# Kernel optimization log

Hardware: AMD Instinct MI355X
Metric: run time of the kernel (lower is better)

## Reference

```python
import jax, jax.numpy as jnp
import numpy as np

K = 2
CAPACITY_FACTOR = 1.25


def setup_inputs() -> dict:
    key = jax.random.key(0)
    ks = jax.random.split(key, 5)
    B, T, D, F, E = 4, 2048, 1024, 4096, 8
    x = jax.random.normal(ks[0], (B, T, D), dtype=jnp.float32)
    w_gate = jax.random.normal(ks[1], (E, D), dtype=jnp.float32) * (1.0 / np.sqrt(D))
    W1 = jax.random.normal(ks[2], (E, F, D), dtype=jnp.float32) * np.sqrt(2.0 / (D + F))
    b1 = jnp.zeros((E, F), dtype=jnp.float32)
    W2 = jax.random.normal(ks[3], (E, D, F), dtype=jnp.float32) * np.sqrt(2.0 / (D + F))
    b2 = jnp.zeros((E, D), dtype=jnp.float32)
    return {"x": x, "w_gate": w_gate, "W1": W1, "b1": b1, "W2": W2, "b2": b2}


def reference(x, w_gate, W1, b1, W2, b2):
    B, T, D = x.shape
    E = w_gate.shape[0]
    S = B * T
    C = int(CAPACITY_FACTOR * S * K / E)  # per-expert capacity
    tokens = x.reshape(S, D)

    # --- routing (fp32 softmax, top-k) ---
    logits = tokens @ w_gate.T                      # [S, E]
    probs = jax.nn.softmax(logits, axis=-1)         # [S, E]
    topk_vals, topk_idx = jax.lax.top_k(probs, K)   # [S, K]

    e_flat = topk_idx.reshape(-1)                   # [S*K] expert id per assignment
    g_flat = topk_vals.reshape(-1)                  # [S*K] gate value
    t_flat = jnp.repeat(jnp.arange(S), K)           # [S*K] source token index

    # --- capacity: position of each assignment within its expert (arrival order) ---
    onehot = jax.nn.one_hot(e_flat, E, dtype=jnp.int32)       # [S*K, E]
    pos = jnp.sum(jnp.cumsum(onehot, axis=0) * onehot, axis=-1) - 1  # [S*K]
    keep = pos < C

    # --- dispatch into [E, C, D] buffer (over-capacity assignments dropped) ---
    buf = jnp.zeros((E, C, D), dtype=tokens.dtype).at[e_flat, pos].set(
        tokens[t_flat], mode="drop")

    # --- grouped expert FFN: fc2(gelu(fc1(x))) + x  (exact gelu, as torch F.gelu) ---
    h = jax.nn.gelu(jnp.einsum("ecd,efd->ecf", buf, W1) + b1[:, None, :],
                    approximate=False)              # [E, C, F]
    expert_out = jnp.einsum("ecf,edf->ecd", h, W2) + b2[:, None, :] + buf  # [E, C, D]

    # --- combine: scatter-add gate-weighted expert outputs back to tokens ---
    gathered = expert_out[e_flat, jnp.clip(pos, 0, C - 1)]    # [S*K, D]
    w = jnp.where(keep, g_flat, 0.0)[:, None]
    y = jnp.zeros((S, D), dtype=tokens.dtype).at[t_flat].add(w * gathered)

    # --- load-balancing aux loss ---
    importance = probs.mean(axis=0)                            # [E]
    counts = jnp.zeros((E,), dtype=probs.dtype).at[e_flat].add(1.0)
    load = counts / S
    aux_loss = E * jnp.sum(importance * load)

    return y.reshape(B, T, D), aux_loss
```

## Files before the change

kernel.cpp:

```cpp
#include <hip/hip_runtime.h>
#include <hip/hip_bf16.h>
#include <math.h>
#include <stdint.h>

#define S_TOK 8192
#define D_DIM 1024
#define F_DIM 4096
#define E_EXP 8
#define C_CAP 2560

typedef __bf16 bf16x8_t __attribute__((ext_vector_type(8)));
typedef __bf16 bf16x4_t __attribute__((ext_vector_type(4)));
typedef float f32x4_t __attribute__((ext_vector_type(4)));

__device__ __forceinline__ void async_copy16(const void* g, void* l) {
  __builtin_amdgcn_global_load_lds(
      (const __attribute__((address_space(1))) unsigned int*)g,
      (__attribute__((address_space(3))) unsigned int*)l, 16, 0, 0);
}

__global__ __launch_bounds__(256) void routing_kernel(
    const float* __restrict__ x, const float* __restrict__ wg,
    __bf16* __restrict__ x_bf, int* __restrict__ asg_e, float* __restrict__ asg_g,
    float* __restrict__ imp_sum)
{
  __shared__ float s_imp[E_EXP];
  const int tid = threadIdx.x, lane = tid & 63, w = tid >> 6;
  if (tid < E_EXP) s_imp[tid] = 0.f;
  __syncthreads();
  const int t = blockIdx.x * 4 + w;

  const float4* xp = (const float4*)(x + (size_t)t * D_DIM);
  float4 xv[4];
#pragma unroll
  for (int j = 0; j < 4; j++) xv[j] = xp[lane + 64 * j];

#pragma unroll
  for (int j = 0; j < 4; j++) {
    bf16x4_t o;
    o[0] = (__bf16)xv[j].x; o[1] = (__bf16)xv[j].y;
    o[2] = (__bf16)xv[j].z; o[3] = (__bf16)xv[j].w;
    *(bf16x4_t*)(x_bf + (size_t)t * D_DIM + (size_t)(lane + 64 * j) * 4) = o;
  }

  float acc[E_EXP];
#pragma unroll
  for (int e = 0; e < E_EXP; e++) acc[e] = 0.f;
#pragma unroll
  for (int e = 0; e < E_EXP; e++) {
    const float4* wp = (const float4*)(wg + (size_t)e * D_DIM);
#pragma unroll
    for (int j = 0; j < 4; j++) {
      const float4 wv = wp[lane + 64 * j];
      acc[e] += xv[j].x * wv.x + xv[j].y * wv.y + xv[j].z * wv.z + xv[j].w * wv.w;
    }
  }
#pragma unroll
  for (int e = 0; e < E_EXP; e++)
    for (int off = 32; off > 0; off >>= 1) acc[e] += __shfl_xor(acc[e], off);

  if (lane == 0) {
    float m = acc[0];
#pragma unroll
    for (int e = 1; e < E_EXP; e++) m = fmaxf(m, acc[e]);
    float p[E_EXP], s = 0.f;
#pragma unroll
    for (int e = 0; e < E_EXP; e++) { p[e] = expf(acc[e] - m); s += p[e]; }
    const float inv = 1.f / s;
#pragma unroll
    for (int e = 0; e < E_EXP; e++) p[e] *= inv;
    int e0 = 0; float v0 = p[0];
#pragma unroll
    for (int e = 1; e < E_EXP; e++) if (p[e] > v0) { v0 = p[e]; e0 = e; }
    int e1 = -1; float v1 = -1.f;
#pragma unroll
    for (int e = 0; e < E_EXP; e++) if (e != e0 && p[e] > v1) { v1 = p[e]; e1 = e; }
    asg_e[2 * t] = e0; asg_g[2 * t] = v0;
    asg_e[2 * t + 1] = e1; asg_g[2 * t + 1] = v1;
#pragma unroll
    for (int e = 0; e < E_EXP; e++) atomicAdd(&s_imp[e], p[e]);
  }
  __syncthreads();
  if (tid < E_EXP) atomicAdd(&imp_sum[tid], s_imp[tid]);
}

__global__ __launch_bounds__(256) void cvt2_kernel(
    const float* __restrict__ s1, const float* __restrict__ s2,
    __bf16* __restrict__ d1, __bf16* __restrict__ d2, int n4each)
{
  const int stride = gridDim.x * blockDim.x;
  for (int i = blockIdx.x * blockDim.x + threadIdx.x; i < 2 * n4each; i += stride) {
    const int half = (i >= n4each);
    const int j = half ? (i - n4each) : i;
    const float4 v = half ? ((const float4*)s2)[j] : ((const float4*)s1)[j];
    bf16x4_t o;
    o[0] = (__bf16)v.x; o[1] = (__bf16)v.y; o[2] = (__bf16)v.z; o[3] = (__bf16)v.w;
    if (half) ((bf16x4_t*)d2)[j] = o; else ((bf16x4_t*)d1)[j] = o;
  }
}

__global__ __launch_bounds__(256) void positions_kernel(
    const int* __restrict__ asg_e, const float* __restrict__ asg_g,
    const float* __restrict__ imp_sum, int* __restrict__ slot_token,
    float* __restrict__ slot_gate, int* __restrict__ cnt_g, float* __restrict__ aux_out)
{
  __shared__ int lcnt[E_EXP * 256];
  __shared__ int tot[E_EXP];
  const int tid = threadIdx.x;
  int cnt[E_EXP];
#pragma unroll
  for (int e = 0; e < E_EXP; e++) cnt[e] = 0;
  const int a0 = tid * 64;
  for (int j = 0; j < 64; j++) {
    const int ae = asg_e[a0 + j];
#pragma unroll
    for (int e = 0; e < E_EXP; e++) cnt[e] += (ae == e) ? 1 : 0;
  }
#pragma unroll
  for (int e = 0; e < E_EXP; e++) lcnt[e * 256 + tid] = cnt[e];
  __syncthreads();
  if (tid < E_EXP) {
    int run = 0;
    for (int i = 0; i < 256; i++) { const int v = lcnt[tid * 256 + i]; lcnt[tid * 256 + i] = run; run += v; }
    tot[tid] = run;
    cnt_g[tid] = run;
  }
  __syncthreads();
  int base[E_EXP];
#pragma unroll
  for (int e = 0; e < E_EXP; e++) base[e] = lcnt[e * 256 + tid];
  for (int j = 0; j < 64; j++) {
    const int a = a0 + j;
    const int ae = asg_e[a];
    int pp = 0;
#pragma unroll
    for (int e = 0; e < E_EXP; e++) {
      if (ae == e) { pp = base[e]; base[e] = pp + 1; }
    }
    if (pp < C_CAP) { slot_token[ae * C_CAP + pp] = a >> 1; slot_gate[ae * C_CAP + pp] = asg_g[a]; }
  }
  if (tid == 0) {
    float aux = 0.f;
#pragma unroll
    for (int e = 0; e < E_EXP; e++) aux += imp_sum[e] * (float)tot[e];
    aux_out[0] = (float)E_EXP * aux / ((float)S_TOK * (float)S_TOK);
  }
}

#define WAIT_VM0 asm volatile("s_waitcnt vmcnt(0)" ::: "memory")

template <int MODE>
__global__ __launch_bounds__(256, 2) void moe_gemm(
    const __bf16* __restrict__ A, const __bf16* __restrict__ Bw,
    const float* __restrict__ bias, const int* __restrict__ slot_token,
    const float* __restrict__ slot_gate, const float* __restrict__ xres,
    const int* __restrict__ cnt, __bf16* __restrict__ Hout, float* __restrict__ y,
    int MT, int NT, int N, int K)
{
  const int ntiles = gridDim.x;
  const int xcd = blockIdx.x & 7, slot = blockIdx.x >> 3;
  const int tile = xcd * (ntiles >> 3) + slot;
  const int e = tile / (MT * NT);
  const int t_ = tile % (MT * NT);
  const int grp = t_ / (4 * NT), rem = t_ % (4 * NT);
  const int mt = grp * 4 + (rem & 3), nt = rem >> 2;
  const int m0 = mt * 128, n0 = nt * 128;
  if (m0 >= cnt[e]) return;

  const int tid = threadIdx.x, lane = tid & 63, w = tid >> 6;
  const int wm = w >> 1, wn = w & 1;

  __shared__ __align__(16) unsigned short sA[2][128][64];
  __shared__ __align__(16) unsigned short sB[2][128][64];

  const int rstage = lane >> 3;
  const int cstage = (lane & 7) ^ rstage;

  const char* gA[4];
  const char* gB[4];
#pragma unroll
  for (int i = 0; i < 4; i++) {
    const int rowA = w * 32 + i * 8 + rstage;
    size_t arow;
    if (MODE == 0) {
      int tok = slot_token[e * C_CAP + m0 + rowA];
      if (tok < 0) tok = 0;
      arow = (size_t)tok * (size_t)K;
    } else {
      arow = ((size_t)(e * C_CAP + m0 + rowA)) * (size_t)K;
    }
    gA[i] = (const char*)(A + arow) + cstage * 16;
    const int rowB = w * 32 + i * 8 + rstage;
    const size_t brow = ((size_t)(e * N + n0 + rowB)) * (size_t)K;
    gB[i] = (const char*)(Bw + brow) + cstage * 16;
  }

#define STAGE(BUF, kt) do {                                                         \
    const size_t koff_ = (size_t)(kt) * 128;                                        \
    _Pragma("unroll")                                                               \
    for (int i_ = 0; i_ < 4; i_++)                                                  \
      async_copy16(gA[i_] + koff_, (void*)&sA[BUF][w * 32 + i_ * 8][0]);            \
    _Pragma("unroll")                                                               \
    for (int i_ = 0; i_ < 4; i_++)                                                  \
      async_copy16(gB[i_] + koff_, (void*)&sB[BUF][w * 32 + i_ * 8][0]);            \
  } while (0)

  f32x4_t acc[4][4];
#pragma unroll
  for (int mi = 0; mi < 4; mi++)
#pragma unroll
    for (int ni = 0; ni < 4; ni++) acc[mi][ni] = (f32x4_t){0.f, 0.f, 0.f, 0.f};

  const int fr = lane & 15;
  const int fq = lane >> 4;

#define COMPUTE(BUF)                                                                \
  _Pragma("unroll")                                                                 \
  for (int kk = 0; kk < 2; kk++) {                                                  \
    bf16x8_t af[4], bfv[4];                                                         \
    _Pragma("unroll")                                                               \
    for (int mi = 0; mi < 4; mi++) {                                                \
      const int row = wm * 64 + mi * 16 + fr;                                       \
      const int chk = (kk * 4 + fq) ^ (row & 7);                                    \
      af[mi] = *(const bf16x8_t*)&sA[BUF][row][chk * 8];                            \
    }                                                                               \
    _Pragma("unroll")                                                               \
    for (int ni = 0; ni < 4; ni++) {                                                \
      const int row = wn * 64 + ni * 16 + fr;                                       \
      const int chk = (kk * 4 + fq) ^ (row & 7);                                    \
      bfv[ni] = *(const bf16x8_t*)&sB[BUF][row][chk * 8];                           \
    }                                                                               \
    __builtin_amdgcn_s_setprio(1);                                                  \
    _Pragma("unroll")                                                               \
    for (int mi = 0; mi < 4; mi++)                                                  \
      _Pragma("unroll")                                                             \
      for (int ni = 0; ni < 4; ni++)                                                \
        acc[mi][ni] = __builtin_amdgcn_mfma_f32_16x16x32_bf16(af[mi], bfv[ni],      \
                                                              acc[mi][ni], 0, 0, 0);\
    __builtin_amdgcn_s_setprio(0);                                                  \
  }

  const int NTILES = K >> 6;
  STAGE(0, 0);
  WAIT_VM0;
  __builtin_amdgcn_s_barrier();

  for (int t = 0; t < NTILES; t += 2) {
    STAGE(1, t + 1);
    COMPUTE(0);
    WAIT_VM0;
    __builtin_amdgcn_s_barrier();
    if (t + 2 < NTILES) {
      STAGE(0, t + 2);
      COMPUTE(1);
      WAIT_VM0;
      __builtin_amdgcn_s_barrier();
    } else {
      COMPUTE(1);
    }
  }

  const int col_lo = lane & 15;
  const int row_hi = (lane >> 4) * 4;
  if (MODE == 0) {
#pragma unroll
    for (int ni = 0; ni < 4; ni++) {
      const int gcol = n0 + wn * 64 + ni * 16 + col_lo;
      const float bv = bias[e * N + gcol];
#pragma unroll
      for (int mi = 0; mi < 4; mi++) {
#pragma unroll
        for (int r = 0; r < 4; r++) {
          const int grow = m0 + wm * 64 + mi * 16 + row_hi + r;
          const float v = acc[mi][ni][r] + bv;
          const float gl = 0.5f * v * (1.0f + erff(v * 0.70710678118654752f));
          Hout[((size_t)(e * C_CAP + grow)) * (size_t)N + gcol] = (__bf16)gl;
        }
      }
    }
  } else {
#pragma unroll
    for (int mi = 0; mi < 4; mi++) {
#pragma unroll
      for (int r = 0; r < 4; r++) {
        const int slotI = e * C_CAP + m0 + wm * 64 + mi * 16 + row_hi + r;
        const int tok = slot_token[slotI];
        if (tok < 0) continue;
        const float g = slot_gate[slotI];
        const size_t trow = (size_t)tok * (size_t)N;
#pragma unroll
        for (int ni = 0; ni < 4; ni++) {
          const int gcol = n0 + wn * 64 + ni * 16 + col_lo;
          const float v = acc[mi][ni][r] + bias[e * N + gcol] + xres[trow + gcol];
          atomicAdd(&y[trow + gcol], g * v);
        }
      }
    }
  }
#undef STAGE
#undef COMPUTE
}

extern "C" void kernel_launch(void* const* d_in, const int* in_sizes, int n_in,
                              void* d_out, int out_size, void* d_ws, size_t ws_size,
                              hipStream_t stream) {
  const float* x  = (const float*)d_in[0];
  const float* wg = (const float*)d_in[1];
  const float* W1 = (const float*)d_in[2];
  const float* b1 = (const float*)d_in[3];
  const float* W2 = (const float*)d_in[4];
  const float* b2 = (const float*)d_in[5];
  float* y = (float*)d_out;

  char* p = (char*)d_ws;
  __bf16* x_bf = (__bf16*)p;    p += (size_t)S_TOK * D_DIM * 2;
  __bf16* w1_bf = (__bf16*)p;   p += (size_t)E_EXP * F_DIM * D_DIM * 2;
  __bf16* w2_bf = (__bf16*)p;   p += (size_t)E_EXP * F_DIM * D_DIM * 2;
  __bf16* Hbuf = (__bf16*)p;    p += (size_t)E_EXP * C_CAP * F_DIM * 2;
  int* slot_token = (int*)p;    p += (size_t)E_EXP * C_CAP * 4;
  float* slot_gate = (float*)p; p += (size_t)E_EXP * C_CAP * 4;
  int* asg_e = (int*)p;         p += (size_t)S_TOK * 2 * 4;
  float* asg_g = (float*)p;     p += (size_t)S_TOK * 2 * 4;
  float* imp_sum = (float*)p;   p += 64;
  int* cnt_g = (int*)p;         p += 64;

  hipMemsetAsync(d_out, 0, ((size_t)S_TOK * D_DIM + 1) * sizeof(float), stream);
  hipMemsetAsync(imp_sum, 0, E_EXP * sizeof(float), stream);
  hipMemsetAsync(slot_token, 0xFF, (size_t)E_EXP * C_CAP * sizeof(int), stream);

  routing_kernel<<<S_TOK / 4, 256, 0, stream>>>(x, wg, x_bf, asg_e, asg_g, imp_sum);
  cvt2_kernel<<<4096, 256, 0, stream>>>(W1, W2, w1_bf, w2_bf, E_EXP * F_DIM * D_DIM / 4);
  positions_kernel<<<1, 256, 0, stream>>>(asg_e, asg_g, imp_sum, slot_token, slot_gate,
                                          cnt_g, y + (size_t)S_TOK * D_DIM);
  moe_gemm<0><<<E_EXP * 20 * 32, 256, 0, stream>>>(x_bf, w1_bf, b1, slot_token, nullptr,
                                                   nullptr, cnt_g, Hbuf, nullptr,
                                                   20, 32, F_DIM, D_DIM);
  moe_gemm<1><<<E_EXP * 20 * 8, 256, 0, stream>>>(Hbuf, w2_bf, b2, slot_token, slot_gate,
                                                  x, cnt_g, nullptr, y,
                                                  20, 8, D_DIM, F_DIM);
}
```

Before: 1.033 ms.

## Enlarge GEMM tiles to 256x256 / 128x256 with 512-thread blocks

Expert GEMMs move to 512-thread blocks (8 waves in a 2x4 grid) with larger output tiles: 256x256 for the FC1 GEMM and 128x256 for the FC2 GEMM. Each wave now keeps up to 8x4 MFMA accumulators, and A fragments are loaded in groups of four to limit register pressure. The tile swizzle groups two M-tiles per N-stripe instead of four, and the grid sizes are reduced to match. The aim is more operand reuse per LDS and global load, at the cost of more LDS (64 KB for FC1), more registers and fewer blocks, which may hurt occupancy and tail balance.

```diff
diff --git a/kernel.cpp b/kernel.cpp
--- a/kernel.cpp
+++ b/kernel.cpp
@@ -150,37 +150,44 @@
 #define WAIT_VM0 asm volatile("s_waitcnt vmcnt(0)" ::: "memory")
 
 template <int MODE>
-__global__ __launch_bounds__(256, 2) void moe_gemm(
+__global__ __launch_bounds__(512, 2) void moe_gemm(
     const __bf16* __restrict__ A, const __bf16* __restrict__ Bw,
     const float* __restrict__ bias, const int* __restrict__ slot_token,
     const float* __restrict__ slot_gate, const float* __restrict__ xres,
     const int* __restrict__ cnt, __bf16* __restrict__ Hout, float* __restrict__ y,
     int MT, int NT, int N, int K)
 {
+  constexpr int BM = (MODE == 0) ? 256 : 128;
+  constexpr int MFRAG = BM / 32;
+  constexpr int MQ = MFRAG / 4;
+  constexpr int AGROUPS = BM / 64;
+
   const int ntiles = gridDim.x;
   const int xcd = blockIdx.x & 7, slot = blockIdx.x >> 3;
   const int tile = xcd * (ntiles >> 3) + slot;
   const int e = tile / (MT * NT);
   const int t_ = tile % (MT * NT);
-  const int grp = t_ / (4 * NT), rem = t_ % (4 * NT);
-  const int mt = grp * 4 + (rem & 3), nt = rem >> 2;
-  const int m0 = mt * 128, n0 = nt * 128;
+  const int grp = t_ / (2 * NT), rem = t_ % (2 * NT);
+  const int mt = grp * 2 + (rem & 1), nt = rem >> 1;
+  const int m0 = mt * BM, n0 = nt * 256;
   if (m0 >= cnt[e]) return;
 
   const int tid = threadIdx.x, lane = tid & 63, w = tid >> 6;
-  const int wm = w >> 1, wn = w & 1;
-
-  __shared__ __align__(16) unsigned short sA[2][128][64];
-  __shared__ __align__(16) unsigned short sB[2][128][64];
+  const int wm = w >> 2, wn = w & 3;
+
+  __shared__ __align__(16) unsigned short sA[2][BM][64];
+  __shared__ __align__(16) unsigned short sB[2][256][64];
 
   const int rstage = lane >> 3;
   const int cstage = (lane & 7) ^ rstage;
-
-  const char* gA[4];
+  const int wArow = w * (BM / 8);
+  const int wBrow = w * 32;
+
+  const char* gA[AGROUPS];
   const char* gB[4];
 #pragma unroll
-  for (int i = 0; i < 4; i++) {
-    const int rowA = w * 32 + i * 8 + rstage;
+  for (int i = 0; i < AGROUPS; i++) {
+    const int rowA = wArow + i * 8 + rstage;
     size_t arow;
     if (MODE == 0) {
       int tok = slot_token[e * C_CAP + m0 + rowA];
@@ -190,24 +197,26 @@
       arow = ((size_t)(e * C_CAP + m0 + rowA)) * (size_t)K;
     }
     gA[i] = (const char*)(A + arow) + cstage * 16;
-    const int rowB = w * 32 + i * 8 + rstage;
-    const size_t brow = ((size_t)(e * N + n0 + rowB)) * (size_t)K;
-    gB[i] = (const char*)(Bw + brow) + cstage * 16;
+  }
+#pragma unroll
+  for (int i = 0; i < 4; i++) {
+    const int rowB = wBrow + i * 8 + rstage;
+    gB[i] = (const char*)(Bw + ((size_t)(e * N + n0 + rowB)) * (size_t)K) + cstage * 16;
   }
 
 #define STAGE(BUF, kt) do {                                                         \
     const size_t koff_ = (size_t)(kt) * 128;                                        \
     _Pragma("unroll")                                                               \
-    for (int i_ = 0; i_ < 4; i_++)                                                  \
-      async_copy16(gA[i_] + koff_, (void*)&sA[BUF][w * 32 + i_ * 8][0]);            \
+    for (int i_ = 0; i_ < AGROUPS; i_++)                                            \
+      async_copy16(gA[i_] + koff_, (void*)&sA[BUF][wArow + i_ * 8][0]);             \
     _Pragma("unroll")                                                               \
     for (int i_ = 0; i_ < 4; i_++)                                                  \
-      async_copy16(gB[i_] + koff_, (void*)&sB[BUF][w * 32 + i_ * 8][0]);            \
+      async_copy16(gB[i_] + koff_, (void*)&sB[BUF][wBrow + i_ * 8][0]);             \
   } while (0)
 
-  f32x4_t acc[4][4];
-#pragma unroll
-  for (int mi = 0; mi < 4; mi++)
+  f32x4_t acc[MFRAG][4];
+#pragma unroll
+  for (int mi = 0; mi < MFRAG; mi++)
 #pragma unroll
     for (int ni = 0; ni < 4; ni++) acc[mi][ni] = (f32x4_t){0.f, 0.f, 0.f, 0.f};
 
@@ -217,27 +226,31 @@
 #define COMPUTE(BUF)                                                                \
   _Pragma("unroll")                                                                 \
   for (int kk = 0; kk < 2; kk++) {                                                  \
-    bf16x8_t af[4], bfv[4];                                                         \
-    _Pragma("unroll")                                                               \
-    for (int mi = 0; mi < 4; mi++) {                                                \
-      const int row = wm * 64 + mi * 16 + fr;                                       \
-      const int chk = (kk * 4 + fq) ^ (row & 7);                                    \
-      af[mi] = *(const bf16x8_t*)&sA[BUF][row][chk * 8];                            \
-    }                                                                               \
+    bf16x8_t bfv[4];                                                                \
     _Pragma("unroll")                                                               \
     for (int ni = 0; ni < 4; ni++) {                                                \
       const int row = wn * 64 + ni * 16 + fr;                                       \
       const int chk = (kk * 4 + fq) ^ (row & 7);                                    \
       bfv[ni] = *(const bf16x8_t*)&sB[BUF][row][chk * 8];                           \
     }                                                                               \
-    __builtin_amdgcn_s_setprio(1);                                                  \
     _Pragma("unroll")                                                               \
-    for (int mi = 0; mi < 4; mi++)                                                  \
+    for (int mh = 0; mh < MQ; mh++) {                                               \
+      bf16x8_t af[4];                                                               \
       _Pragma("unroll")                                                             \
-      for (int ni = 0; ni < 4; ni++)                                                \
-        acc[mi][ni] = __builtin_amdgcn_mfma_f32_16x16x32_bf16(af[mi], bfv[ni],      \
-                                                              acc[mi][ni], 0, 0, 0);\
-    __builtin_amdgcn_s_setprio(0);                                                  \
+      for (int mi = 0; mi < 4; mi++) {                                              \
+        const int row = wm * (BM / 2) + (mh * 4 + mi) * 16 + fr;                    \
+        const int chk = (kk * 4 + fq) ^ (row & 7);                                  \
+        af[mi] = *(const bf16x8_t*)&sA[BUF][row][chk * 8];                          \
+      }                                                                             \
+      __builtin_amdgcn_s_setprio(1);                                                \
+      _Pragma("unroll")                                                             \
+      for (int mi = 0; mi < 4; mi++)                                                \
+        _Pragma("unroll")                                                           \
+        for (int ni = 0; ni < 4; ni++)                                              \
+          acc[mh * 4 + mi][ni] = __builtin_amdgcn_mfma_f32_16x16x32_bf16(           \
+              af[mi], bfv[ni], acc[mh * 4 + mi][ni], 0, 0, 0);                      \
+      __builtin_amdgcn_s_setprio(0);                                                \
+    }                                                                               \
   }
 
   const int NTILES = K >> 6;
@@ -268,10 +281,10 @@
       const int gcol = n0 + wn * 64 + ni * 16 + col_lo;
       const float bv = bias[e * N + gcol];
 #pragma unroll
-      for (int mi = 0; mi < 4; mi++) {
+      for (int mi = 0; mi < MFRAG; mi++) {
 #pragma unroll
         for (int r = 0; r < 4; r++) {
-          const int grow = m0 + wm * 64 + mi * 16 + row_hi + r;
+          const int grow = m0 + wm * (BM / 2) + mi * 16 + row_hi + r;
           const float v = acc[mi][ni][r] + bv;
           const float gl = 0.5f * v * (1.0f + erff(v * 0.70710678118654752f));
           Hout[((size_t)(e * C_CAP + grow)) * (size_t)N + gcol] = (__bf16)gl;
@@ -280,10 +293,10 @@
     }
   } else {
 #pragma unroll
-    for (int mi = 0; mi < 4; mi++) {
+    for (int mi = 0; mi < MFRAG; mi++) {
 #pragma unroll
       for (int r = 0; r < 4; r++) {
-        const int slotI = e * C_CAP + m0 + wm * 64 + mi * 16 + row_hi + r;
+        const int slotI = e * C_CAP + m0 + wm * (BM / 2) + mi * 16 + row_hi + r;
         const int tok = slot_token[slotI];
         if (tok < 0) continue;
         const float g = slot_gate[slotI];
@@ -332,10 +345,10 @@
   cvt2_kernel<<<4096, 256, 0, stream>>>(W1, W2, w1_bf, w2_bf, E_EXP * F_DIM * D_DIM / 4);
   positions_kernel<<<1, 256, 0, stream>>>(asg_e, asg_g, imp_sum, slot_token, slot_gate,
                                           cnt_g, y + (size_t)S_TOK * D_DIM);
-  moe_gemm<0><<<E_EXP * 20 * 32, 256, 0, stream>>>(x_bf, w1_bf, b1, slot_token, nullptr,
+  moe_gemm<0><<<E_EXP * 10 * 16, 512, 0, stream>>>(x_bf, w1_bf, b1, slot_token, nullptr,
                                                    nullptr, cnt_g, Hbuf, nullptr,
-                                                   20, 32, F_DIM, D_DIM);
-  moe_gemm<1><<<E_EXP * 20 * 8, 256, 0, stream>>>(Hbuf, w2_bf, b2, slot_token, slot_gate,
+                                                   10, 16, F_DIM, D_DIM);
+  moe_gemm<1><<<E_EXP * 20 * 4, 512, 0, stream>>>(Hbuf, w2_bf, b2, slot_token, slot_gate,
                                                   x, cnt_g, nullptr, y,
-                                                  20, 8, D_DIM, F_DIM);
-}
+                                                  20, 4, D_DIM, F_DIM);
+}
```

New measurement: 1.635 ms. +58.4%, slower.
